# Kernel optimization log

Hardware: AMD Instinct MI355X
Metric: run time of the kernel (lower is better)

The kernel has to match this reference:

```python
import jax, jax.numpy as jnp
import numpy as np

B, S, E, D, DE = 8, 128, 50, 300, 50  # batch, seq, edge_dim, gcn_dim, dep_embed_dim
EPS = 1e-6


def setup_inputs() -> dict:
    key = jax.random.key(0)
    ks = jax.random.split(key, 9)
    weight_prob_softmax = jax.nn.softmax(jax.random.normal(ks[0], (B, S, S, E)), axis=2)
    weight_adj = jax.random.normal(ks[1], (B, S, S, E))
    gcn_inputs = jax.random.normal(ks[2], (B, S, D))
    # self-loop added to adjacency after permute -> [B, E, S, S]; identity loops
    self_loop = jnp.broadcast_to(jnp.eye(S, dtype=jnp.float32), (B, E, S, S))
    W_w = jax.random.normal(ks[3], (D, D)) * 0.05          # gcn linear (in, out)
    W_b = jnp.zeros((D,))
    ln_a = jnp.ones((D,))
    ln_b = jnp.zeros((D,))
    refine_W = jax.random.normal(ks[4], (2 * D + 3 * E, DE)) * 0.05  # (750, 50)
    refine_b = jnp.zeros((DE,))
    return {
        "weight_prob_softmax": weight_prob_softmax,
        "weight_adj": weight_adj,
        "gcn_inputs": gcn_inputs,
        "self_loop": self_loop,
        "W_w": W_w, "W_b": W_b,
        "ln_a": ln_a, "ln_b": ln_b,
        "refine_W": refine_W, "refine_b": refine_b,
    }


def reference(weight_prob_softmax, weight_adj, gcn_inputs, self_loop,
              W_w, W_b, ln_a, ln_b, refine_W, refine_b):
    b, s, d = gcn_inputs.shape
    e = weight_prob_softmax.shape[-1]
    # [B,S,S,E] -> [B,E,S,S], add self loops
    wps = jnp.transpose(weight_prob_softmax, (0, 3, 1, 2)) + self_loop
    # per-relation-channel message passing: Ax[b,e,i,:] = sum_j wps[b,e,i,j] * x[b,j,:]
    Ax = jnp.einsum('beij,bjd->beid', wps, gcn_inputs)
    Ax = Ax.mean(axis=1)  # avg pooling over edge channels -> [B,S,D]
    h = Ax @ W_w + W_b
    # LayerNorm with unbiased std (torch x.std default) and (std + eps)
    mean = h.mean(axis=-1, keepdims=True)
    var_unbiased = jnp.sum((h - mean) ** 2, axis=-1, keepdims=True) / (d - 1)
    std = jnp.sqrt(var_unbiased)
    h = ln_a * (h - mean) / (std + EPS) + ln_b
    node = jax.nn.relu(h)  # [B,S,D]
    # node1[b,i,j] = node[b,j]; node2[b,i,j] = node[b,i]
    node1 = jnp.broadcast_to(node[:, None, :, :], (b, s, s, d))
    node2 = jnp.broadcast_to(node[:, :, None, :], (b, s, s, d))
    # diagonal edge features: [B,E,S] -> [B,S,E]
    diag = jnp.transpose(jnp.diagonal(weight_adj, axis1=1, axis2=2), (0, 2, 1))
    edge_i = jnp.broadcast_to(diag[:, None, :, :], (b, s, s, e))  # edge_i[b,i,j]=diag[b,j]
    edge_j = jnp.broadcast_to(diag[:, :, None, :], (b, s, s, e))  # edge_j[b,i,j]=diag[b,i]
    feat = jnp.concatenate([weight_adj, edge_i, edge_j, node1, node2], axis=-1)
    edge_out = feat @ refine_W + refine_b  # [B,S,S,DE]
    return node, edge_out
```

## Files before the change

kernel.cpp:

```cpp
#include <hip/hip_runtime.h>
#include <hip/hip_bf16.h>


typedef __bf16 bf16x8 __attribute__((ext_vector_type(8)));
typedef float f32x4 __attribute__((ext_vector_type(4)));
typedef float f32x2 __attribute__((ext_vector_type(2)));
typedef float f32x4_u __attribute__((ext_vector_type(4))) __attribute__((aligned(4)));

__device__ __forceinline__ unsigned short f2bf(float f) {
    __hip_bfloat16 h = __float2bfloat16(f);
    union { __hip_bfloat16 h; unsigned short u; } c; c.h = h; return c.u;
}

__device__ __forceinline__ bf16x8 fragA(const float* __restrict__ ap, int e0) {
    union { bf16x8 v; unsigned short u[8]; } c;
    if (e0 <= 40) {
        f32x4_u v0 = *(const f32x4_u*)(ap + e0);
        f32x4_u v1 = *(const f32x4_u*)(ap + e0 + 4);
#pragma unroll
        for (int i = 0; i < 4; ++i) { c.u[i] = f2bf(v0[i]); c.u[4 + i] = f2bf(v1[i]); }
    } else if (e0 == 48) {
        c.u[0] = f2bf(ap[48]); c.u[1] = f2bf(ap[49]);
#pragma unroll
        for (int i = 2; i < 8; ++i) c.u[i] = 0;
    } else {
#pragma unroll
        for (int i = 0; i < 8; ++i) c.u[i] = 0;
    }
    return c.v;
}

__global__ void __launch_bounds__(1024, 8) k_node(
    const float* __restrict__ wps,
    const float* __restrict__ wa,
    const float* __restrict__ x,
    const float* __restrict__ Ww,
    const float* __restrict__ Wb,
    const float* __restrict__ lna,
    const float* __restrict__ lnb,
    const float* __restrict__ Rw,
    const float* __restrict__ rb,
    float* __restrict__ node_out,
    float* __restrict__ R1, float* __restrict__ R2,
    unsigned short* __restrict__ rwPre)
{
    __shared__ __align__(16) float axp[6400];
    __shared__ __align__(16) float axm2[608];
    __shared__ __align__(16) float Mlt[256];
    __shared__ __align__(16) float srcL[704];
    __shared__ float red1[10], red2[10], stats[4];

    int tid = threadIdx.x;
    int row0 = blockIdx.x * 2;
    int b = row0 >> 7, i0 = row0 & 127;

    if (blockIdx.x == 511) {
        for (int idx = tid; idx < 4608; idx += 1024) {
            int kk = idx / 72, e = idx % 72;
            rwPre[idx] = (kk < 50 && e < 50) ? f2bf(Rw[e * 50 + kk]) : (unsigned short)0;
        }
    }

    {
        const float2* p2 = (const float2*)(wps + (size_t)row0 * 6400);
        for (int idx = tid; idx < 6400; idx += 1024) {
            float2 v = p2[idx];
            axp[idx] = v.x + v.y;
        }
    }
    if (tid < 100) {
        int r = tid / 50, e = tid % 50;
        srcL[e * 2 + r] = wa[((size_t)(row0 + r) * 128 + (i0 + r)) * 50 + e];
    }
    __syncthreads();
    if (tid < 256) {
        int r = tid >> 7, j = tid & 127;
        const float* pp = &axp[tid * 25];
        float s = 0.f;
#pragma unroll
        for (int n = 0; n < 25; ++n) s += pp[n];
        Mlt[j * 2 + r] = s * (1.0f / 50.0f) + (((i0 + r) == j) ? 1.0f : 0.0f);
    }
    __syncthreads();

    int t = tid & 255, g = tid >> 8;
    bool has2 = (t < 44);
    int d1 = has2 ? 256 + t : 299;

    {
        f32x2 a0 = {0.f, 0.f}, a1 = {0.f, 0.f};
        const float* xp = x + (size_t)b * 38400;
        int j0 = g * 32;
#pragma unroll 8
        for (int jj = 0; jj < 32; ++jj) {
            int j = j0 + jj;
            f32x2 m2 = *(const f32x2*)&Mlt[j * 2];
            a0 += m2 * xp[j * 300 + t];
            a1 += m2 * xp[j * 300 + d1];
        }
        *(f32x2*)&axp[g * 608 + t * 2] = a0;
        if (has2) *(f32x2*)&axp[g * 608 + d1 * 2] = a1;
    }
    __syncthreads();
    if (tid < 300) {
        f32x2 s = *(f32x2*)&axp[tid * 2]        + *(f32x2*)&axp[608 + tid * 2]
                + *(f32x2*)&axp[1216 + tid * 2] + *(f32x2*)&axp[1824 + tid * 2];
        *(f32x2*)&axm2[tid * 2] = s;
    }
    __syncthreads();

    {
        f32x2 h0 = {0.f, 0.f}, h1 = {0.f, 0.f};
        int kb = g * 75, ke = kb + 75;
#pragma unroll 5
        for (int k = kb; k < ke; ++k) {
            f32x2 m2 = *(const f32x2*)&axm2[k * 2];
            h0 += m2 * Ww[k * 300 + t];
            h1 += m2 * Ww[k * 300 + d1];
        }
        *(f32x2*)&axp[g * 608 + t * 2] = h0;
        if (has2) *(f32x2*)&axp[g * 608 + d1 * 2] = h1;
    }
    __syncthreads();

    f32x2 hv = {0.f, 0.f};
    int wvi = tid >> 6, lane = tid & 63;
    if (tid < 320) {
        if (tid < 300) {
            hv = *(f32x2*)&axp[tid * 2]        + *(f32x2*)&axp[608 + tid * 2]
               + *(f32x2*)&axp[1216 + tid * 2] + *(f32x2*)&axp[1824 + tid * 2];
            hv += Wb[tid];
        }
        float s1r[2], s2r[2];
#pragma unroll
        for (int r = 0; r < 2; ++r) { s1r[r] = hv[r]; s2r[r] = hv[r] * hv[r]; }
        for (int off = 32; off; off >>= 1) {
#pragma unroll
            for (int r = 0; r < 2; ++r) {
                s1r[r] += __shfl_down(s1r[r], off);
                s2r[r] += __shfl_down(s2r[r], off);
            }
        }
        if (lane == 0) {
#pragma unroll
            for (int r = 0; r < 2; ++r) { red1[wvi * 2 + r] = s1r[r]; red2[wvi * 2 + r] = s2r[r]; }
        }
    }
    __syncthreads();
    if (tid < 2) {
        float s1 = 0.f, s2 = 0.f;
#pragma unroll
        for (int w = 0; w < 5; ++w) { s1 += red1[w * 2 + tid]; s2 += red2[w * 2 + tid]; }
        float mean = s1 * (1.0f / 300.0f);
        float var = (s2 - 300.0f * mean * mean) * (1.0f / 299.0f);
        var = fmaxf(var, 0.0f);
        stats[tid * 2] = mean;
        stats[tid * 2 + 1] = 1.0f / (sqrtf(var) + 1e-6f);
    }
    __syncthreads();

    if (tid < 300) {
        float la = lna[tid], lb = lnb[tid];
        f32x2 nv;
#pragma unroll
        for (int r = 0; r < 2; ++r) {
            float v = la * (hv[r] - stats[r * 2]) * stats[r * 2 + 1] + lb;
            v = fmaxf(v, 0.f);
            nv[r] = v;
            node_out[(size_t)(row0 + r) * 300 + tid] = v;
        }
        *(f32x2*)&srcL[(50 + tid) * 2] = nv;
    }
    __syncthreads();

    if (tid < 700) {
        int p = tid / 50, k = tid % 50;
        f32x2 r1a = {0.f, 0.f}, r2a = {0.f, 0.f};
        int ib = p * 25;
#pragma unroll 5
        for (int idx = ib; idx < ib + 25; ++idx) {
            f32x2 sv = *(const f32x2*)&srcL[idx * 2];
            float w1, w2;
            if (idx < 50) { w1 = Rw[(50 + idx) * 50 + k]; w2 = Rw[(100 + idx) * 50 + k]; }
            else { int d = idx - 50; w1 = Rw[(150 + d) * 50 + k]; w2 = Rw[(450 + d) * 50 + k]; }
            r1a += sv * w1;
            r2a += sv * w2;
        }
        *(f32x2*)&axp[(p * 50 + k) * 2] = r1a;
        *(f32x2*)&axp[2800 + (p * 50 + k) * 2] = r2a;
    }
    __syncthreads();
    if (tid < 100) {
        int r = tid / 50, k = tid % 50;
        float s1 = 0.f, s2 = rb[k];
#pragma unroll
        for (int p = 0; p < 14; ++p) {
            s1 += axp[(p * 50 + k) * 2 + r];
            s2 += axp[2800 + (p * 50 + k) * 2 + r];
        }
        R1[(size_t)(row0 + r) * 50 + k] = s1;
        R2[(size_t)(row0 + r) * 50 + k] = s2;
    }
}

__global__ void __launch_bounds__(256) k_edge(
    const float* __restrict__ wa,
    const unsigned int* __restrict__ rwPre,
    const float* __restrict__ R1, const float* __restrict__ R2,
    float* __restrict__ eout)
{
    __shared__ __align__(16) unsigned char smem[25600];
    unsigned short* rwBT = (unsigned short*)smem;
    float* outF = (float*)smem;
    int tid = threadIdx.x;
    int bi = blockIdx.x;
    int b = bi >> 7;

    for (int idx = tid; idx < 2304; idx += 256)
        ((unsigned int*)rwBT)[idx] = rwPre[idx];
    __syncthreads();

    int lane = tid & 63, wv = tid >> 6;
    int q = lane >> 4, lr = lane & 15;
    const float* wab = wa + (size_t)bi * 6400;
    f32x4 acc[2][4] = {};

#pragma unroll
    for (int mi = 0; mi < 2; ++mi) {
        const float* ap = wab + (wv * 32 + mi * 16 + lr) * 50;
#pragma unroll
        for (int ks = 0; ks < 2; ++ks) {
            int e0 = ks * 32 + q * 8;
            bf16x8 a = fragA(ap, e0);
#pragma unroll
            for (int nt = 0; nt < 4; ++nt) {
                bf16x8 bb = *(const bf16x8*)&rwBT[(nt * 16 + lr) * 72 + e0];
                acc[mi][nt] = __builtin_amdgcn_mfma_f32_16x16x32_bf16(a, bb, acc[mi][nt], 0, 0, 0);
            }
        }
    }
    __syncthreads();

    const float* r2p = R2 + (size_t)bi * 50;
#pragma unroll
    for (int nt = 0; nt < 4; ++nt) {
        int kk = nt * 16 + lr;
        if (kk < 50) {
            float r2v = r2p[kk];
#pragma unroll
            for (int mi = 0; mi < 2; ++mi) {
                int jbase = wv * 32 + mi * 16 + q * 4;
#pragma unroll
                for (int r = 0; r < 4; ++r)
                    outF[(jbase + r) * 50 + kk] = acc[mi][nt][r] + r2v;
            }
        }
    }
    __syncthreads();

    const float4* R1b = (const float4*)(R1 + (size_t)b * 6400);
    const float4* L4  = (const float4*)outF;
    float4* op4 = (float4*)(eout + (size_t)bi * 6400);
    for (int f4 = tid; f4 < 1600; f4 += 256) {
        float4 v = L4[f4];
        float4 r = R1b[f4];
        v.x += r.x; v.y += r.y; v.z += r.z; v.w += r.w;
        op4[f4] = v;
    }
}

extern "C" void kernel_launch(void* const* d_in, const int* in_sizes, int n_in,
                              void* d_out, int out_size, void* d_ws, size_t ws_size,
                              hipStream_t stream)
{
    const float* wps = (const float*)d_in[0];
    const float* wa  = (const float*)d_in[1];
    const float* x   = (const float*)d_in[2];
    const float* Ww  = (const float*)d_in[4];
    const float* Wb  = (const float*)d_in[5];
    const float* lna = (const float*)d_in[6];
    const float* lnb = (const float*)d_in[7];
    const float* Rw  = (const float*)d_in[8];
    const float* rb  = (const float*)d_in[9];

    float* R1 = (float*)d_ws;
    float* R2 = ((float*)d_ws) + 51200;
    unsigned short* rwPre16 = (unsigned short*)(((float*)d_ws) + 102400);
    const unsigned int* rwPre32 = (const unsigned int*)rwPre16;

    float* node_out = (float*)d_out;
    float* edge_out = node_out + 307200;

    k_node<<<512, 1024, 0, stream>>>(wps, wa, x, Ww, Wb, lna, lnb, Rw, rb,
                                     node_out, R1, R2, rwPre16);
    k_edge<<<1024, 256, 0, stream>>>(wa, rwPre32, R1, R2, edge_out);
}
```

Baseline: 153.8 us.

## Split node path into prep kernel plus bf16 MFMA node kernel

Replaces the fp32 scalar node kernel with a prep kernel that reduces the softmax weights to a bf16 adjacency matrix and transposes x, Ww and the refine weights into bf16 layouts. A new 64-block kernel then does Ax, the linear layer, LayerNorm and the R1/R2 projections with 16x16x32 bf16 MFMA instructions, processing 16 rows per block. The goal is to move the node GEMMs onto matrix cores and cut per-block redundant weight traffic. In exchange it adds an extra launch and a workspace round-trip, uses fewer blocks (only 64), and lowers intermediate precision to bf16.

```diff
diff --git a/kernel.cpp b/kernel.cpp
--- a/kernel.cpp
+++ b/kernel.cpp
@@ -4,13 +4,198 @@
 
 typedef __bf16 bf16x8 __attribute__((ext_vector_type(8)));
 typedef float f32x4 __attribute__((ext_vector_type(4)));
-typedef float f32x2 __attribute__((ext_vector_type(2)));
-typedef float f32x4_u __attribute__((ext_vector_type(4))) __attribute__((aligned(4)));
 
 __device__ __forceinline__ unsigned short f2bf(float f) {
     __hip_bfloat16 h = __float2bfloat16(f);
     union { __hip_bfloat16 h; unsigned short u; } c; c.h = h; return c.u;
 }
+
+__global__ void __launch_bounds__(256) k_prep(
+    const float* __restrict__ wps,
+    const float* __restrict__ x,
+    const float* __restrict__ Ww,
+    const float* __restrict__ Rw,
+    unsigned short* __restrict__ Mbf,
+    unsigned short* __restrict__ xT,
+    unsigned short* __restrict__ WwT,
+    unsigned short* __restrict__ RW2T,
+    unsigned short* __restrict__ rwPre)
+{
+    int tid = threadIdx.x, blk = blockIdx.x;
+    int row0 = blk * 2;
+    int i0 = row0 & 127;
+
+    {
+        int r = tid >> 7, j = tid & 127;
+        const float2* p2 = (const float2*)(wps + ((size_t)(row0 + r) * 128 + j) * 50);
+        float s = 0.f;
+#pragma unroll
+        for (int n = 0; n < 25; ++n) { float2 v = p2[n]; s += v.x + v.y; }
+        float m = s * (1.0f / 50.0f) + (((i0 + r) == j) ? 1.0f : 0.0f);
+        Mbf[(size_t)(row0 + r) * 128 + j] = f2bf(m);
+    }
+
+    if (blk < 64) {
+        int bb = blk >> 3, j0 = (blk & 7) * 16;
+        const float* xb = x + (size_t)bb * 38400;
+        for (int el = tid; el < 4800; el += 256) {
+            int j = j0 + el / 300, d = el % 300;
+            xT[((size_t)bb * 304 + d) * 128 + j] = f2bf(xb[j * 300 + d]);
+        }
+        if (tid < 64) {
+            int d = 300 + (tid >> 4), j = j0 + (tid & 15);
+            xT[((size_t)bb * 304 + d) * 128 + j] = 0;
+        }
+    } else if (blk < 140) {
+        int d0 = (blk - 64) * 4;
+        for (int el = tid; el < 1280; el += 256) {
+            int d = d0 + el / 320, k = el % 320;
+            unsigned short v = 0;
+            if (d < 300 && k < 300) v = f2bf(Ww[k * 300 + d]);
+            WwT[d * 320 + k] = v;
+        }
+    } else if (blk < 168) {
+        int r0 = (blk - 140) * 4;
+        for (int el = tid; el < 1408; el += 256) {
+            int row = r0 + el / 352, idx = el % 352;
+            unsigned short v = 0;
+            if (row < 50) {
+                if (idx < 50)       v = f2bf(Rw[(50 + idx) * 50 + row]);
+                else if (idx < 350) v = f2bf(Rw[(150 + idx - 50) * 50 + row]);
+            } else if (row < 100) {
+                int q = row - 50;
+                if (idx < 50)       v = f2bf(Rw[(100 + idx) * 50 + q]);
+                else if (idx < 350) v = f2bf(Rw[(450 + idx - 50) * 50 + q]);
+            }
+            RW2T[row * 352 + idx] = v;
+        }
+    } else if (blk == 200) {
+        for (int idx = tid; idx < 4608; idx += 256) {
+            int kk = idx / 72, e = idx % 72;
+            rwPre[idx] = (kk < 50 && e < 50) ? f2bf(Rw[e * 50 + kk]) : (unsigned short)0;
+        }
+    }
+}
+
+__global__ void __launch_bounds__(256) k_node_mfma(
+    const unsigned short* __restrict__ Mbf,
+    const unsigned short* __restrict__ xT,
+    const unsigned short* __restrict__ WwT,
+    const unsigned short* __restrict__ RW2T,
+    const float* __restrict__ wa,
+    const float* __restrict__ Wb,
+    const float* __restrict__ lna,
+    const float* __restrict__ lnb,
+    const float* __restrict__ rb,
+    float* __restrict__ node_out,
+    float* __restrict__ R1, float* __restrict__ R2)
+{
+    __shared__ __align__(16) unsigned short a2bf[16 * 344];
+    __shared__ __align__(16) float hL[16 * 308];
+    __shared__ __align__(16) unsigned short srcbf[16 * 360];
+
+    int tid = threadIdx.x;
+    int b = blockIdx.x >> 3, i0 = (blockIdx.x & 7) * 16;
+    int brow = b * 128 + i0;
+    int lane = tid & 63, wv = tid >> 6;
+    int q = lane >> 4, lr = lane & 15;
+
+    for (int i = tid; i < 640; i += 256) { int m = i / 40; a2bf[m * 344 + 304 + i % 40] = 0; }
+    if (tid < 160) { int m = tid / 10; srcbf[m * 360 + 350 + tid % 10] = 0; }
+    for (int i = tid; i < 800; i += 256) {
+        int m = i / 50, e = i % 50;
+        srcbf[m * 360 + e] = f2bf(wa[((size_t)(brow + m) * 128 + (i0 + m)) * 50 + e]);
+    }
+
+    bf16x8 A1[4];
+#pragma unroll
+    for (int ks = 0; ks < 4; ++ks)
+        A1[ks] = *(const bf16x8*)&Mbf[(size_t)(brow + lr) * 128 + ks * 32 + q * 8];
+    for (int nt = wv; nt < 19; nt += 4) {
+        f32x4 acc = {0.f, 0.f, 0.f, 0.f};
+#pragma unroll
+        for (int ks = 0; ks < 4; ++ks) {
+            bf16x8 bb = *(const bf16x8*)&xT[((size_t)b * 304 + nt * 16 + lr) * 128 + ks * 32 + q * 8];
+            acc = __builtin_amdgcn_mfma_f32_16x16x32_bf16(A1[ks], bb, acc, 0, 0, 0);
+        }
+#pragma unroll
+        for (int r = 0; r < 4; ++r)
+            a2bf[(q * 4 + r) * 344 + nt * 16 + lr] = f2bf(acc[r]);
+    }
+    __syncthreads();
+
+    bf16x8 A2[10];
+#pragma unroll
+    for (int ks = 0; ks < 10; ++ks)
+        A2[ks] = *(const bf16x8*)&a2bf[lr * 344 + ks * 32 + q * 8];
+    for (int nt = wv; nt < 19; nt += 4) {
+        f32x4 acc = {0.f, 0.f, 0.f, 0.f};
+#pragma unroll
+        for (int ks = 0; ks < 10; ++ks) {
+            bf16x8 bb = *(const bf16x8*)&WwT[(size_t)(nt * 16 + lr) * 320 + ks * 32 + q * 8];
+            acc = __builtin_amdgcn_mfma_f32_16x16x32_bf16(A2[ks], bb, acc, 0, 0, 0);
+        }
+        int n = nt * 16 + lr;
+        float wbv = (n < 300) ? Wb[n] : 0.f;
+#pragma unroll
+        for (int r = 0; r < 4; ++r)
+            hL[(q * 4 + r) * 308 + n] = (n < 300) ? (acc[r] + wbv) : 0.f;
+    }
+    __syncthreads();
+
+    {
+        int trow = tid >> 4, c = tid & 15;
+        float s1 = 0.f, s2 = 0.f;
+#pragma unroll
+        for (int kk = 0; kk < 19; ++kk) {
+            float v = hL[trow * 308 + c + kk * 16];
+            s1 += v; s2 += v * v;
+        }
+#pragma unroll
+        for (int off = 1; off < 16; off <<= 1) {
+            s1 += __shfl_xor(s1, off);
+            s2 += __shfl_xor(s2, off);
+        }
+        float mean = s1 * (1.0f / 300.0f);
+        float var = (s2 - 300.0f * mean * mean) * (1.0f / 299.0f);
+        var = fmaxf(var, 0.0f);
+        float rstd = 1.0f / (sqrtf(var) + 1e-6f);
+        float* nrow = node_out + (size_t)(brow + trow) * 300;
+#pragma unroll
+        for (int kk = 0; kk < 19; ++kk) {
+            int n = c + kk * 16;
+            if (n < 300) {
+                float v = lna[n] * (hL[trow * 308 + n] - mean) * rstd + lnb[n];
+                v = fmaxf(v, 0.f);
+                nrow[n] = v;
+                srcbf[trow * 360 + 50 + n] = f2bf(v);
+            }
+        }
+    }
+    __syncthreads();
+
+    bf16x8 A3[11];
+#pragma unroll
+    for (int ks = 0; ks < 11; ++ks)
+        A3[ks] = *(const bf16x8*)&srcbf[lr * 360 + ks * 32 + q * 8];
+    for (int nt = wv; nt < 7; nt += 4) {
+        f32x4 acc = {0.f, 0.f, 0.f, 0.f};
+#pragma unroll
+        for (int ks = 0; ks < 11; ++ks) {
+            bf16x8 bb = *(const bf16x8*)&RW2T[(size_t)(nt * 16 + lr) * 352 + ks * 32 + q * 8];
+            acc = __builtin_amdgcn_mfma_f32_16x16x32_bf16(A3[ks], bb, acc, 0, 0, 0);
+        }
+        int qq = nt * 16 + lr;
+#pragma unroll
+        for (int r = 0; r < 4; ++r) {
+            int m = q * 4 + r;
+            if (qq < 50)       R1[(size_t)(brow + m) * 50 + qq] = acc[r];
+            else if (qq < 100) R2[(size_t)(brow + m) * 50 + qq - 50] = acc[r] + rb[qq - 50];
+        }
+    }
+}
+
+typedef float f32x4_u __attribute__((ext_vector_type(4))) __attribute__((aligned(4)));
 
 __device__ __forceinline__ bf16x8 fragA(const float* __restrict__ ap, int e0) {
     union { bf16x8 v; unsigned short u[8]; } c;
@@ -28,179 +213,6 @@
         for (int i = 0; i < 8; ++i) c.u[i] = 0;
     }
     return c.v;
-}
-
-__global__ void __launch_bounds__(1024, 8) k_node(
-    const float* __restrict__ wps,
-    const float* __restrict__ wa,
-    const float* __restrict__ x,
-    const float* __restrict__ Ww,
-    const float* __restrict__ Wb,
-    const float* __restrict__ lna,
-    const float* __restrict__ lnb,
-    const float* __restrict__ Rw,
-    const float* __restrict__ rb,
-    float* __restrict__ node_out,
-    float* __restrict__ R1, float* __restrict__ R2,
-    unsigned short* __restrict__ rwPre)
-{
-    __shared__ __align__(16) float axp[6400];
-    __shared__ __align__(16) float axm2[608];
-    __shared__ __align__(16) float Mlt[256];
-    __shared__ __align__(16) float srcL[704];
-    __shared__ float red1[10], red2[10], stats[4];
-
-    int tid = threadIdx.x;
-    int row0 = blockIdx.x * 2;
-    int b = row0 >> 7, i0 = row0 & 127;
-
-    if (blockIdx.x == 511) {
-        for (int idx = tid; idx < 4608; idx += 1024) {
-            int kk = idx / 72, e = idx % 72;
-            rwPre[idx] = (kk < 50 && e < 50) ? f2bf(Rw[e * 50 + kk]) : (unsigned short)0;
-        }
-    }
-
-    {
-        const float2* p2 = (const float2*)(wps + (size_t)row0 * 6400);
-        for (int idx = tid; idx < 6400; idx += 1024) {
-            float2 v = p2[idx];
-            axp[idx] = v.x + v.y;
-        }
-    }
-    if (tid < 100) {
-        int r = tid / 50, e = tid % 50;
-        srcL[e * 2 + r] = wa[((size_t)(row0 + r) * 128 + (i0 + r)) * 50 + e];
-    }
-    __syncthreads();
-    if (tid < 256) {
-        int r = tid >> 7, j = tid & 127;
-        const float* pp = &axp[tid * 25];
-        float s = 0.f;
-#pragma unroll
-        for (int n = 0; n < 25; ++n) s += pp[n];
-        Mlt[j * 2 + r] = s * (1.0f / 50.0f) + (((i0 + r) == j) ? 1.0f : 0.0f);
-    }
-    __syncthreads();
-
-    int t = tid & 255, g = tid >> 8;
-    bool has2 = (t < 44);
-    int d1 = has2 ? 256 + t : 299;
-
-    {
-        f32x2 a0 = {0.f, 0.f}, a1 = {0.f, 0.f};
-        const float* xp = x + (size_t)b * 38400;
-        int j0 = g * 32;
-#pragma unroll 8
-        for (int jj = 0; jj < 32; ++jj) {
-            int j = j0 + jj;
-            f32x2 m2 = *(const f32x2*)&Mlt[j * 2];
-            a0 += m2 * xp[j * 300 + t];
-            a1 += m2 * xp[j * 300 + d1];
-        }
-        *(f32x2*)&axp[g * 608 + t * 2] = a0;
-        if (has2) *(f32x2*)&axp[g * 608 + d1 * 2] = a1;
-    }
-    __syncthreads();
-    if (tid < 300) {
-        f32x2 s = *(f32x2*)&axp[tid * 2]        + *(f32x2*)&axp[608 + tid * 2]
-                + *(f32x2*)&axp[1216 + tid * 2] + *(f32x2*)&axp[1824 + tid * 2];
-        *(f32x2*)&axm2[tid * 2] = s;
-    }
-    __syncthreads();
-
-    {
-        f32x2 h0 = {0.f, 0.f}, h1 = {0.f, 0.f};
-        int kb = g * 75, ke = kb + 75;
-#pragma unroll 5
-        for (int k = kb; k < ke; ++k) {
-            f32x2 m2 = *(const f32x2*)&axm2[k * 2];
-            h0 += m2 * Ww[k * 300 + t];
-            h1 += m2 * Ww[k * 300 + d1];
-        }
-        *(f32x2*)&axp[g * 608 + t * 2] = h0;
-        if (has2) *(f32x2*)&axp[g * 608 + d1 * 2] = h1;
-    }
-    __syncthreads();
-
-    f32x2 hv = {0.f, 0.f};
-    int wvi = tid >> 6, lane = tid & 63;
-    if (tid < 320) {
-        if (tid < 300) {
-            hv = *(f32x2*)&axp[tid * 2]        + *(f32x2*)&axp[608 + tid * 2]
-               + *(f32x2*)&axp[1216 + tid * 2] + *(f32x2*)&axp[1824 + tid * 2];
-            hv += Wb[tid];
-        }
-        float s1r[2], s2r[2];
-#pragma unroll
-        for (int r = 0; r < 2; ++r) { s1r[r] = hv[r]; s2r[r] = hv[r] * hv[r]; }
-        for (int off = 32; off; off >>= 1) {
-#pragma unroll
-            for (int r = 0; r < 2; ++r) {
-                s1r[r] += __shfl_down(s1r[r], off);
-                s2r[r] += __shfl_down(s2r[r], off);
-            }
-        }
-        if (lane == 0) {
-#pragma unroll
-            for (int r = 0; r < 2; ++r) { red1[wvi * 2 + r] = s1r[r]; red2[wvi * 2 + r] = s2r[r]; }
-        }
-    }
-    __syncthreads();
-    if (tid < 2) {
-        float s1 = 0.f, s2 = 0.f;
-#pragma unroll
-        for (int w = 0; w < 5; ++w) { s1 += red1[w * 2 + tid]; s2 += red2[w * 2 + tid]; }
-        float mean = s1 * (1.0f / 300.0f);
-        float var = (s2 - 300.0f * mean * mean) * (1.0f / 299.0f);
-        var = fmaxf(var, 0.0f);
-        stats[tid * 2] = mean;
-        stats[tid * 2 + 1] = 1.0f / (sqrtf(var) + 1e-6f);
-    }
-    __syncthreads();
-
-    if (tid < 300) {
-        float la = lna[tid], lb = lnb[tid];
-        f32x2 nv;
-#pragma unroll
-        for (int r = 0; r < 2; ++r) {
-            float v = la * (hv[r] - stats[r * 2]) * stats[r * 2 + 1] + lb;
-            v = fmaxf(v, 0.f);
-            nv[r] = v;
-            node_out[(size_t)(row0 + r) * 300 + tid] = v;
-        }
-        *(f32x2*)&srcL[(50 + tid) * 2] = nv;
-    }
-    __syncthreads();
-
-    if (tid < 700) {
-        int p = tid / 50, k = tid % 50;
-        f32x2 r1a = {0.f, 0.f}, r2a = {0.f, 0.f};
-        int ib = p * 25;
-#pragma unroll 5
-        for (int idx = ib; idx < ib + 25; ++idx) {
-            f32x2 sv = *(const f32x2*)&srcL[idx * 2];
-            float w1, w2;
-            if (idx < 50) { w1 = Rw[(50 + idx) * 50 + k]; w2 = Rw[(100 + idx) * 50 + k]; }
-            else { int d = idx - 50; w1 = Rw[(150 + d) * 50 + k]; w2 = Rw[(450 + d) * 50 + k]; }
-            r1a += sv * w1;
-            r2a += sv * w2;
-        }
-        *(f32x2*)&axp[(p * 50 + k) * 2] = r1a;
-        *(f32x2*)&axp[2800 + (p * 50 + k) * 2] = r2a;
-    }
-    __syncthreads();
-    if (tid < 100) {
-        int r = tid / 50, k = tid % 50;
-        float s1 = 0.f, s2 = rb[k];
-#pragma unroll
-        for (int p = 0; p < 14; ++p) {
-            s1 += axp[(p * 50 + k) * 2 + r];
-            s2 += axp[2800 + (p * 50 + k) * 2 + r];
-        }
-        R1[(size_t)(row0 + r) * 50 + k] = s1;
-        R2[(size_t)(row0 + r) * 50 + k] = s2;
-    }
 }
 
 __global__ void __launch_bounds__(256) k_edge(
@@ -283,15 +295,20 @@
     const float* Rw  = (const float*)d_in[8];
     const float* rb  = (const float*)d_in[9];
 
-    float* R1 = (float*)d_ws;
-    float* R2 = ((float*)d_ws) + 51200;
-    unsigned short* rwPre16 = (unsigned short*)(((float*)d_ws) + 102400);
-    const unsigned int* rwPre32 = (const unsigned int*)rwPre16;
+    float* wsf = (float*)d_ws;
+    float* R1 = wsf;
+    float* R2 = wsf + 51200;
+    unsigned short* rwPre16 = (unsigned short*)(wsf + 102400);
+    unsigned short* Mbf  = (unsigned short*)(wsf + 104704);
+    unsigned short* xT   = (unsigned short*)(wsf + 170240);
+    unsigned short* WwT  = (unsigned short*)(wsf + 325888);
+    unsigned short* RW2T = (unsigned short*)(wsf + 374528);
 
     float* node_out = (float*)d_out;
     float* edge_out = node_out + 307200;
 
-    k_node<<<512, 1024, 0, stream>>>(wps, wa, x, Ww, Wb, lna, lnb, Rw, rb,
-                                     node_out, R1, R2, rwPre16);
-    k_edge<<<1024, 256, 0, stream>>>(wa, rwPre32, R1, R2, edge_out);
-}
+    k_prep<<<512, 256, 0, stream>>>(wps, x, Ww, Rw, Mbf, xT, WwT, RW2T, rwPre16);
+    k_node_mfma<<<64, 256, 0, stream>>>(Mbf, xT, WwT, RW2T, wa, Wb, lna, lnb, rb,
+                                        node_out, R1, R2);
+    k_edge<<<1024, 256, 0, stream>>>(wa, (const unsigned int*)rwPre16, R1, R2, edge_out);
+}
```

Measured after the change: 157.2 us. 2.2% more time.
